# Kernel tuning notes

Measured on AMD Instinct MI355X. Metric: run time of the kernel, lower is better.

Reference implementation:

```python
import jax, jax.numpy as jnp
import numpy as np

N_NODES = 100000
N_EDGES = 1600000
EMB = 64       # embedding_dim
HID = 128      # hidden_channels
N_GRAPHS = 512
N_TASKS = 128
ATOM_VOCAB = 119
BOND_VOCAB = 16


def setup_inputs() -> dict:
    key = jax.random.key(0)
    ks = jax.random.split(key, 24)
    s = 0.02
    inp = {
        'x_idx': jax.random.randint(ks[0], (N_NODES,), 0, ATOM_VOCAB),
        'edge_index': jax.random.randint(ks[1], (2, N_EDGES), 0, N_NODES),
        'edge_attr_idx': jax.random.randint(ks[2], (N_EDGES,), 0, BOND_VOCAB),
        'batch': jnp.sort(jax.random.randint(ks[3], (N_NODES,), 0, N_GRAPHS)),
        'atom_emb': jax.random.normal(ks[4], (ATOM_VOCAB, EMB), jnp.float32) * s,
        'bond_emb': jax.random.normal(ks[5], (BOND_VOCAB, EMB), jnp.float32) * s,
        'w_edge0': jax.random.normal(ks[6], (EMB, EMB), jnp.float32) * s,
        'b_edge0': jnp.zeros((EMB,), jnp.float32),
        'w1_0': jax.random.normal(ks[7], (EMB, HID), jnp.float32) * s,
        'b1_0': jnp.zeros((HID,), jnp.float32),
        'w2_0': jax.random.normal(ks[8], (HID, HID), jnp.float32) * s,
        'b2_0': jnp.zeros((HID,), jnp.float32),
        'w_edge1': jax.random.normal(ks[9], (EMB, HID), jnp.float32) * s,
        'b_edge1': jnp.zeros((HID,), jnp.float32),
        'w1_1': jax.random.normal(ks[10], (HID, HID), jnp.float32) * s,
        'b1_1': jnp.zeros((HID,), jnp.float32),
        'w2_1': jax.random.normal(ks[11], (HID, HID), jnp.float32) * s,
        'b2_1': jnp.zeros((HID,), jnp.float32),
        'lin1_w': jax.random.normal(ks[12], (HID, HID), jnp.float32) * s,
        'lin1_b': jnp.zeros((HID,), jnp.float32),
        'lin2_w': jax.random.normal(ks[13], (HID, N_TASKS), jnp.float32) * s,
        'lin2_b': jnp.zeros((N_TASKS,), jnp.float32),
    }
    return inp


def _gine_conv(x, e, src, dst, we, be, w1, b1, w2, b2):
    # message: relu(x_j + Linear(edge_attr)); aggregate: scatter-add at dst
    msg = jax.nn.relu(x[src] + e @ we + be)            # [E, in_dim]
    agg = jax.ops.segment_sum(msg, dst, num_segments=N_NODES)
    h = x + agg                                        # (1+eps)*x with eps=0
    h = jax.nn.elu(h @ w1 + b1) @ w2 + b2              # GINE nn MLP
    return jax.nn.elu(h)                               # outer F.elu


def reference(x_idx, edge_index, edge_attr_idx, batch,
              atom_emb, bond_emb,
              w_edge0, b_edge0, w1_0, b1_0, w2_0, b2_0,
              w_edge1, b_edge1, w1_1, b1_1, w2_1, b2_1,
              lin1_w, lin1_b, lin2_w, lin2_b):
    x = atom_emb[x_idx]                                # [N, EMB]
    e = bond_emb[edge_attr_idx]                        # [E, EMB]
    src, dst = edge_index[0], edge_index[1]            # flow: source->target
    x = _gine_conv(x, e, src, dst, w_edge0, b_edge0, w1_0, b1_0, w2_0, b2_0)
    x = _gine_conv(x, e, src, dst, w_edge1, b_edge1, w1_1, b1_1, w2_1, b2_1)
    hg = jax.ops.segment_sum(x, batch, num_segments=N_GRAPHS)  # global_add_pool
    hg = jax.nn.relu(hg @ lin1_w + lin1_b)
    return hg @ lin2_w + lin2_b                        # [G, num_tasks]
```

## Files before the change

### kernel.cpp

```cpp
#include <hip/hip_runtime.h>
#include <hip/hip_bf16.h>

static const int NN = 100000;
static const int NE = 1600000;
static const int NG = 512;
static const int NB = 391;
static const int PS = 4608;
static const int CS = 4624;

typedef __attribute__((ext_vector_type(8))) short shortx8;
typedef __attribute__((ext_vector_type(4))) float floatx4;
typedef __attribute__((ext_vector_type(2))) float floatx2;

__device__ __forceinline__ float bf2f(unsigned short u) {
  union { unsigned int i; float f; } v; v.i = ((unsigned int)u) << 16; return v.f;
}
__device__ __forceinline__ unsigned short f2bf(float f) {
  union { float f; unsigned int i; } v; v.f = f;
  return (unsigned short)((v.i + 0x7FFFu + ((v.i >> 16) & 1u)) >> 16);
}
__device__ __forceinline__ float elu_fast(float v) {
  return v > 0.f ? v : (__builtin_amdgcn_exp2f(v * 1.44269504f) - 1.f);
}
__device__ __forceinline__ floatx2 unpk(unsigned int v) {
  union { unsigned int i; float f; } a, b;
  a.i = v << 16; b.i = v & 0xFFFF0000u;
  floatx2 r; r.x = a.f; r.y = b.f; return r;
}

__global__ void k_prep(const float* __restrict__ bond,
                       const float* __restrict__ we0, const float* __restrict__ be0,
                       const float* __restrict__ we1, const float* __restrict__ be1,
                       const float* __restrict__ atom,
                       float* __restrict__ et1, unsigned short* __restrict__ M0,
                       float* __restrict__ hgf, int* __restrict__ bcursor,
                       const float* __restrict__ s0, const float* __restrict__ s1,
                       const float* __restrict__ s2, const float* __restrict__ s3,
                       const float* __restrict__ s4, const float* __restrict__ s5,
                       unsigned short* __restrict__ d0, unsigned short* __restrict__ d1,
                       unsigned short* __restrict__ d2, unsigned short* __restrict__ d3,
                       unsigned short* __restrict__ d4, unsigned short* __restrict__ d5) {
  int blk = blockIdx.x, t = threadIdx.x;
  if (blk < 8) {
    int i = blk * 256 + t;
    int b = i >> 7, c = i & 127;
    float acc = be1[c];
    for (int k = 0; k < 64; ++k) acc += bond[b * 64 + k] * we1[k * 128 + c];
    et1[i] = acc;
  } else if (blk < 484) {
    int i = (blk - 8) * 256 + t;
    int c = i & 63, b = (i >> 6) & 15, a = i >> 10;
    float acc = be0[c];
    for (int k = 0; k < 64; ++k) acc += bond[b * 64 + k] * we0[k * 64 + c];
    acc += atom[a * 64 + c];
    M0[i] = f2bf(acc > 0.f ? acc : 0.f);
  } else if (blk < 868) {
    int task = (blk - 484) >> 6;
    int i = ((blk - 484) & 63) * 256 + t;
    const float* w; unsigned short* wz; int K;
    switch (task) {
      case 0: w = s0; wz = d0; K = 64; break;
      case 1: w = s1; wz = d1; K = 128; break;
      case 2: w = s2; wz = d2; K = 128; break;
      case 3: w = s3; wz = d3; K = 128; break;
      case 4: w = s4; wz = d4; K = 128; break;
      default: w = s5; wz = d5; K = 128; break;
    }
    if (i >= K * 128) return;
    int j = i & 7, lane = (i >> 3) & 63, ct = (i >> 9) & 7, s = i >> 12;
    int k = s * 32 + (lane >> 4) * 8 + j;
    int m = ct * 16 + (lane & 15);
    wz[i] = f2bf(w[k * 128 + m]);
  } else if (blk < 884) {
    int base = (blk - 868) * 4096;
#pragma unroll
    for (int k = 0; k < 16; ++k) hgf[base + k * 256 + t] = 0.f;
  } else {
    if (t < NB) bcursor[t] = t * PS;
    int u = t + 256;
    if (u < NB) bcursor[u] = u * PS;
  }
}

__global__ void k_bin(const int* __restrict__ src, const int* __restrict__ dstp,
                      const int* __restrict__ ea, const int* __restrict__ x_idx,
                      int* __restrict__ bcursor, uint2* __restrict__ pairs) {
  __shared__ int cnt[512];
  __shared__ int incl[512];
  __shared__ int cur[NB];
  __shared__ int rbase[NB];
  __shared__ uint2 stage[4096];
  int t = threadIdx.x;
  int e0 = blockIdx.x * 4096;
  int ecnt = NE - e0; if (ecnt > 4096) ecnt = 4096;
  cnt[t] = 0; cnt[t + 256] = 0;
  __syncthreads();
  for (int k = 0; k < 16; ++k) {
    int i = k * 256 + t;
    if (i < ecnt) atomicAdd(&cnt[dstp[e0 + i] >> 8], 1);
  }
  __syncthreads();
  incl[t] = cnt[t]; incl[t + 256] = cnt[t + 256];
  __syncthreads();
  for (int d = 1; d < 512; d <<= 1) {
    int v0 = (t >= d) ? incl[t - d] : 0;
    int v1 = (t + 256 >= d) ? incl[t + 256 - d] : 0;
    __syncthreads();
    incl[t] += v0; incl[t + 256] += v1;
    __syncthreads();
  }
  if (t < NB) { cur[t] = incl[t] - cnt[t]; if (cnt[t]) rbase[t] = atomicAdd(&bcursor[t], cnt[t]); }
  int u = t + 256;
  if (u < NB) { cur[u] = incl[u] - cnt[u]; if (cnt[u]) rbase[u] = atomicAdd(&bcursor[u], cnt[u]); }
  __syncthreads();
  for (int k = 0; k < 16; ++k) {
    int i = k * 256 + t;
    if (i < ecnt) {
      int e = e0 + i;
      int d = dstp[e];
      int s = src[e];
      unsigned int pk = (unsigned int)s | ((unsigned int)(x_idx[s] * 16 + ea[e]) << 17);
      int p = atomicAdd(&cur[d >> 8], 1);
      stage[p] = make_uint2((unsigned int)d, pk);
    }
  }
  __syncthreads();
  for (int j = t; j < ecnt; j += 256) {
    uint2 p = stage[j];
    int b = (int)(p.x >> 8);
    int excl = incl[b] - cnt[b];
    pairs[rbase[b] + (j - excl)] = p;
  }
}

__global__ void k_fine(const uint2* __restrict__ pairs, const int* __restrict__ bcursor,
                       int* __restrict__ offs, int* __restrict__ cnts,
                       unsigned int* __restrict__ csr0, unsigned int* __restrict__ csr1) {
  __shared__ int cnt[256];
  __shared__ int incl[256];
  __shared__ int cur[256];
  int b = blockIdx.x;
  int t = threadIdx.x;
  int start = b * PS;
  int endv = bcursor[b];
  int cbase = b * CS;
  int base_n = b << 8;
  cnt[t] = 0;
  __syncthreads();
  for (int j = start + t; j < endv; j += 256)
    atomicAdd(&cnt[(int)pairs[j].x - base_n], 1);
  __syncthreads();
  incl[t] = cnt[t];
  __syncthreads();
  for (int d = 1; d < 256; d <<= 1) {
    int v = (t >= d) ? incl[t - d] : 0;
    __syncthreads();
    incl[t] += v;
    __syncthreads();
  }
  int excl = incl[t] - cnt[t];
  cur[t] = excl;
  int node = base_n + t;
  if (node < NN) { offs[node] = cbase + excl; cnts[node] = cnt[t]; }
  __syncthreads();
  for (int j = start + t; j < endv; j += 256) {
    uint2 p = pairs[j];
    int pos = cbase + atomicAdd(&cur[(int)p.x - base_n], 1);
    unsigned int pk = p.y;
    unsigned int idx17 = pk >> 17;
    csr0[pos] = idx17 << 7;
    csr1[pos] = ((pk & 0x1FFFFu) << 8) | (idx17 & 15u);
  }
  __syncthreads();
  int total = incl[255];
  if (t < 16) { csr0[cbase + total + t] = 0u; csr1[cbase + total + t] = 0u; }
}

__global__ __launch_bounds__(256) void k_agg0(
    const int* __restrict__ x_idx, const float* __restrict__ atom,
    const unsigned short* __restrict__ M0, const int* __restrict__ offs,
    const int* __restrict__ cnts,
    const unsigned int* __restrict__ csr0, unsigned short* __restrict__ h0) {
  int t = threadIdx.x, lane = t & 63;
  int half = lane >> 5, c = lane & 31;
  int n = __builtin_amdgcn_readfirstlane(blockIdx.x * 4 + (t >> 6));
  if (n >= NN) return;
  int s = offs[n], e = s + cnts[n];
  const char* Mb = (const char*)M0;
  unsigned int voff = (unsigned int)c * 4u;
  floatx2 acc; acc.x = 0.f; acc.y = 0.f;
  if (half == 0) {
    float2 sv = *(const float2*)((const char*)atom +
                                 ((size_t)(unsigned)x_idx[n] << 8) + (size_t)c * 8u);
    acc.x = sv.x; acc.y = sv.y;
  }
  for (int i = s; i < e; i += 16) {
    unsigned int a0 = csr0[i + 0],  b0 = csr0[i + 1];
    unsigned int a1 = csr0[i + 2],  b1 = csr0[i + 3];
    unsigned int a2 = csr0[i + 4],  b2 = csr0[i + 5];
    unsigned int a3 = csr0[i + 6],  b3 = csr0[i + 7];
    unsigned int a4 = csr0[i + 8],  b4 = csr0[i + 9];
    unsigned int a5 = csr0[i + 10], b5 = csr0[i + 11];
    unsigned int a6 = csr0[i + 12], b6 = csr0[i + 13];
    unsigned int a7 = csr0[i + 14], b7 = csr0[i + 15];
    unsigned int q0 = half ? b0 : a0, q1 = half ? b1 : a1;
    unsigned int q2 = half ? b2 : a2, q3 = half ? b3 : a3;
    unsigned int q4 = half ? b4 : a4, q5 = half ? b5 : a5;
    unsigned int q6 = half ? b6 : a6, q7 = half ? b7 : a7;
    floatx2 m0, m1, m2, m3, m4, m5, m6, m7;
    m0.x = m0.y = (i + 0 + half < e) ? 1.f : 0.f;
    m1.x = m1.y = (i + 2 + half < e) ? 1.f : 0.f;
    m2.x = m2.y = (i + 4 + half < e) ? 1.f : 0.f;
    m3.x = m3.y = (i + 6 + half < e) ? 1.f : 0.f;
    m4.x = m4.y = (i + 8 + half < e) ? 1.f : 0.f;
    m5.x = m5.y = (i + 10 + half < e) ? 1.f : 0.f;
    m6.x = m6.y = (i + 12 + half < e) ? 1.f : 0.f;
    m7.x = m7.y = (i + 14 + half < e) ? 1.f : 0.f;
    unsigned int v0 = *(const unsigned int*)(Mb + q0 + voff);
    unsigned int v1 = *(const unsigned int*)(Mb + q1 + voff);
    unsigned int v2 = *(const unsigned int*)(Mb + q2 + voff);
    unsigned int v3 = *(const unsigned int*)(Mb + q3 + voff);
    unsigned int v4 = *(const unsigned int*)(Mb + q4 + voff);
    unsigned int v5 = *(const unsigned int*)(Mb + q5 + voff);
    unsigned int v6 = *(const unsigned int*)(Mb + q6 + voff);
    unsigned int v7 = *(const unsigned int*)(Mb + q7 + voff);
    acc = __builtin_elementwise_fma(m0, unpk(v0), acc);
    acc = __builtin_elementwise_fma(m1, unpk(v1), acc);
    acc = __builtin_elementwise_fma(m2, unpk(v2), acc);
    acc = __builtin_elementwise_fma(m3, unpk(v3), acc);
    acc = __builtin_elementwise_fma(m4, unpk(v4), acc);
    acc = __builtin_elementwise_fma(m5, unpk(v5), acc);
    acc = __builtin_elementwise_fma(m6, unpk(v6), acc);
    acc = __builtin_elementwise_fma(m7, unpk(v7), acc);
  }
  float ax = acc.x + __shfl_xor(acc.x, 32);
  float ay = acc.y + __shfl_xor(acc.y, 32);
  if (half == 0) {
    unsigned int o = (unsigned int)f2bf(ax) | ((unsigned int)f2bf(ay) << 16);
    *(unsigned int*)(h0 + (size_t)n * 64 + c * 2) = o;
  }
}

__global__ __launch_bounds__(256) void k_agg1(
    const unsigned short* __restrict__ x1, const float* __restrict__ et1,
    const int* __restrict__ offs, const int* __restrict__ cnts,
    const unsigned int* __restrict__ csr1, unsigned short* __restrict__ h1) {
  __shared__ float etl[2048];
  int t = threadIdx.x;
#pragma unroll
  for (int k = 0; k < 8; ++k) etl[k * 256 + t] = et1[k * 256 + t];
  __syncthreads();
  int lane = t & 63;
  int n = __builtin_amdgcn_readfirstlane(blockIdx.x * 4 + (t >> 6));
  if (n >= NN) return;
  int s = offs[n], e = s + cnts[n];
  const char* xb = (const char*)x1;
  unsigned int voff = (unsigned int)lane * 4u;
  const char* etb = (const char*)etl + (size_t)lane * 8u;
  unsigned int xv = *(const unsigned int*)(xb + ((size_t)(unsigned)n << 8) + voff);
  floatx2 acc = unpk(xv);
  floatx2 zero2; zero2.x = 0.f; zero2.y = 0.f;
  for (int i = s; i < e; i += 8) {
    unsigned int q0 = csr1[i + 0], q1 = csr1[i + 1], q2 = csr1[i + 2], q3 = csr1[i + 3];
    unsigned int q4 = csr1[i + 4], q5 = csr1[i + 5], q6 = csr1[i + 6], q7 = csr1[i + 7];
    floatx2 k1, k2, k3, k4, k5, k6, k7;
    k1.x = k1.y = (i + 1 < e) ? 1.f : 0.f;
    k2.x = k2.y = (i + 2 < e) ? 1.f : 0.f;
    k3.x = k3.y = (i + 3 < e) ? 1.f : 0.f;
    k4.x = k4.y = (i + 4 < e) ? 1.f : 0.f;
    k5.x = k5.y = (i + 5 < e) ? 1.f : 0.f;
    k6.x = k6.y = (i + 6 < e) ? 1.f : 0.f;
    k7.x = k7.y = (i + 7 < e) ? 1.f : 0.f;
    unsigned int v0 = *(const unsigned int*)(xb + (q0 & 0xFFFFFF00u) + voff);
    unsigned int v1 = *(const unsigned int*)(xb + (q1 & 0xFFFFFF00u) + voff);
    unsigned int v2 = *(const unsigned int*)(xb + (q2 & 0xFFFFFF00u) + voff);
    unsigned int v3 = *(const unsigned int*)(xb + (q3 & 0xFFFFFF00u) + voff);
    unsigned int v4 = *(const unsigned int*)(xb + (q4 & 0xFFFFFF00u) + voff);
    unsigned int v5 = *(const unsigned int*)(xb + (q5 & 0xFFFFFF00u) + voff);
    unsigned int v6 = *(const unsigned int*)(xb + (q6 & 0xFFFFFF00u) + voff);
    unsigned int v7 = *(const unsigned int*)(xb + (q7 & 0xFFFFFF00u) + voff);
    floatx2 e0 = *(const floatx2*)(etb + ((q0 & 15u) << 9));
    floatx2 e1 = *(const floatx2*)(etb + ((q1 & 15u) << 9));
    floatx2 e2 = *(const floatx2*)(etb + ((q2 & 15u) << 9));
    floatx2 e3 = *(const floatx2*)(etb + ((q3 & 15u) << 9));
    floatx2 e4 = *(const floatx2*)(etb + ((q4 & 15u) << 9));
    floatx2 e5 = *(const floatx2*)(etb + ((q5 & 15u) << 9));
    floatx2 e6 = *(const floatx2*)(etb + ((q6 & 15u) << 9));
    floatx2 e7 = *(const floatx2*)(etb + ((q7 & 15u) << 9));
    acc = acc + __builtin_elementwise_max(unpk(v0) + e0, zero2);
    acc = __builtin_elementwise_fma(k1, __builtin_elementwise_max(unpk(v1) + e1, zero2), acc);
    acc = __builtin_elementwise_fma(k2, __builtin_elementwise_max(unpk(v2) + e2, zero2), acc);
    acc = __builtin_elementwise_fma(k3, __builtin_elementwise_max(unpk(v3) + e3, zero2), acc);
    acc = __builtin_elementwise_fma(k4, __builtin_elementwise_max(unpk(v4) + e4, zero2), acc);
    acc = __builtin_elementwise_fma(k5, __builtin_elementwise_max(unpk(v5) + e5, zero2), acc);
    acc = __builtin_elementwise_fma(k6, __builtin_elementwise_max(unpk(v6) + e6, zero2), acc);
    acc = __builtin_elementwise_fma(k7, __builtin_elementwise_max(unpk(v7) + e7, zero2), acc);
  }
  unsigned int o = (unsigned int)f2bf(acc.x) | ((unsigned int)f2bf(acc.y) << 16);
  *(unsigned int*)(h1 + (size_t)n * 128 + lane * 2) = o;
}

template <int K1>
__global__ __launch_bounds__(256) void k_mlp_t(
    const unsigned short* __restrict__ in,
    const unsigned short* __restrict__ w1z, const float* __restrict__ b1,
    const unsigned short* __restrict__ w2z, const float* __restrict__ b2,
    unsigned short* __restrict__ outb, int N) {
  __shared__ unsigned short tls[4][16][136];
  __shared__ unsigned short b2s[16384];
  int t = threadIdx.x;
  int lane = t & 63;
  int wave = t >> 6;
  int rlo = lane & 15, quad = lane >> 4;

#pragma unroll
  for (int k = 0; k < 8; ++k)
    *(shortx8*)&b2s[(k * 256 + t) * 8] = *(const shortx8*)&w2z[(k * 256 + t) * 8];

  float bm1[8], bm2[8];
#pragma unroll
  for (int ct = 0; ct < 8; ++ct) { bm1[ct] = b1[ct * 16 + rlo]; bm2[ct] = b2[ct * 16 + rlo]; }

  __syncthreads();

#pragma unroll
  for (int t2 = 0; t2 < 2; ++t2) {
    int row0 = blockIdx.x * 128 + t2 * 64 + wave * 16;
    int arow = row0 + rlo;

    floatx4 acc[8];
#pragma unroll
    for (int ct = 0; ct < 8; ++ct) { acc[ct][0]=0.f; acc[ct][1]=0.f; acc[ct][2]=0.f; acc[ct][3]=0.f; }
    const int NS = K1 >> 5;
#pragma unroll
    for (int s = 0; s < NS; ++s) {
      shortx8 a = {0,0,0,0,0,0,0,0};
      if (arow < N) a = *(const shortx8*)(in + (size_t)arow * K1 + s * 32 + quad * 8);
      const unsigned short* wp = w1z + ((size_t)(s * 8) * 64 + lane) * 8;
#pragma unroll
      for (int ct = 0; ct < 8; ++ct) {
        shortx8 b = *(const shortx8*)(wp + ct * 512);
        acc[ct] = __builtin_amdgcn_mfma_f32_16x16x32_bf16(a, b, acc[ct], 0, 0, 0);
      }
    }
#pragma unroll
    for (int ct = 0; ct < 8; ++ct) {
#pragma unroll
      for (int r = 0; r < 4; ++r) {
        float v = elu_fast(acc[ct][r] + bm1[ct]);
        tls[wave][quad * 4 + r][ct * 16 + rlo] = f2bf(v);
      }
    }

    floatx4 acc2[8];
#pragma unroll
    for (int ct = 0; ct < 8; ++ct) { acc2[ct][0]=0.f; acc2[ct][1]=0.f; acc2[ct][2]=0.f; acc2[ct][3]=0.f; }
#pragma unroll
    for (int s = 0; s < 4; ++s) {
      shortx8 a = *(const shortx8*)&tls[wave][rlo][s * 32 + quad * 8];
      const unsigned short* wp = &b2s[((s * 8) * 64 + lane) * 8];
#pragma unroll
      for (int ct = 0; ct < 8; ++ct) {
        shortx8 b = *(const shortx8*)(wp + ct * 512);
        acc2[ct] = __builtin_amdgcn_mfma_f32_16x16x32_bf16(a, b, acc2[ct], 0, 0, 0);
      }
    }
#pragma unroll
    for (int ct = 0; ct < 8; ++ct) {
#pragma unroll
      for (int r = 0; r < 4; ++r) {
        float v = elu_fast(acc2[ct][r] + bm2[ct]);
        tls[wave][quad * 4 + r][ct * 16 + rlo] = f2bf(v);
      }
    }
    int srow = lane >> 2;
    int schunk = lane & 3;
    int grow = row0 + srow;
#pragma unroll
    for (int k = 0; k < 4; ++k) {
      int ch = schunk + k * 4;
      if (grow < N)
        *(shortx8*)(outb + (size_t)grow * 128 + ch * 8) =
            *(const shortx8*)&tls[wave][srow][ch * 8];
    }
  }
}

__global__ __launch_bounds__(256) void k_pool(
    const unsigned short* __restrict__ x2, const int* __restrict__ batch,
    float* __restrict__ hgf) {
  int gt = blockIdx.x * 256 + threadIdx.x;
  int chunk = gt >> 6, lane = gt & 63;
  int n0 = chunk * 32;
  if (n0 >= NN) return;
  int nend = n0 + 32; if (nend > NN) nend = NN;
  float ax = 0.f, ay = 0.f;
  const unsigned short* xp = x2 + lane * 2;
  int gcur = batch[n0];
  for (int n = n0; n < nend; ++n) {
    int g = batch[n];
    if (g != gcur) {
      atomicAdd(&hgf[gcur * 128 + lane * 2], ax);
      atomicAdd(&hgf[gcur * 128 + lane * 2 + 1], ay);
      ax = 0.f; ay = 0.f; gcur = g;
    }
    unsigned int v = *(const unsigned int*)(xp + (size_t)n * 128);
    ax += bf2f((unsigned short)(v & 0xFFFF));
    ay += bf2f((unsigned short)(v >> 16));
  }
  atomicAdd(&hgf[gcur * 128 + lane * 2], ax);
  atomicAdd(&hgf[gcur * 128 + lane * 2 + 1], ay);
}

__global__ void k_head(const float* __restrict__ in,
                       const unsigned short* __restrict__ w1z, const float* __restrict__ b1,
                       const unsigned short* __restrict__ w2z, const float* __restrict__ b2,
                       float* __restrict__ outf, int N) {
  __shared__ unsigned short tls[4][16][136];
  int lane = threadIdx.x & 63;
  int wave = threadIdx.x >> 6;
  int row0 = blockIdx.x * 64 + wave * 16;
  int rlo = lane & 15, quad = lane >> 4;
  int arow = row0 + rlo;
  floatx4 acc[8];
#pragma unroll
  for (int ct = 0; ct < 8; ++ct) { acc[ct][0]=0.f; acc[ct][1]=0.f; acc[ct][2]=0.f; acc[ct][3]=0.f; }
#pragma unroll
  for (int s = 0; s < 4; ++s) {
    shortx8 a = {0,0,0,0,0,0,0,0};
    if (arow < N) {
      const float* rp = in + (size_t)arow * 128 + s * 32 + quad * 8;
      float4 f0 = *(const float4*)rp;
      float4 f1 = *(const float4*)(rp + 4);
      a[0] = (short)f2bf(f0.x); a[1] = (short)f2bf(f0.y);
      a[2] = (short)f2bf(f0.z); a[3] = (short)f2bf(f0.w);
      a[4] = (short)f2bf(f1.x); a[5] = (short)f2bf(f1.y);
      a[6] = (short)f2bf(f1.z); a[7] = (short)f2bf(f1.w);
    }
    const unsigned short* wp = w1z + ((size_t)(s * 8) * 64 + lane) * 8;
#pragma unroll
    for (int ct = 0; ct < 8; ++ct) {
      shortx8 b = *(const shortx8*)(wp + ct * 512);
      acc[ct] = __builtin_amdgcn_mfma_f32_16x16x32_bf16(a, b, acc[ct], 0, 0, 0);
    }
  }
#pragma unroll
  for (int ct = 0; ct < 8; ++ct) {
    float bm = b1[ct * 16 + rlo];
#pragma unroll
    for (int r = 0; r < 4; ++r) {
      float v = acc[ct][r] + bm;
      v = v > 0.f ? v : 0.f;
      tls[wave][quad * 4 + r][ct * 16 + rlo] = f2bf(v);
    }
  }
  __syncthreads();
  floatx4 acc2[8];
#pragma unroll
  for (int ct = 0; ct < 8; ++ct) { acc2[ct][0]=0.f; acc2[ct][1]=0.f; acc2[ct][2]=0.f; acc2[ct][3]=0.f; }
#pragma unroll
  for (int s = 0; s < 4; ++s) {
    shortx8 a = *(const shortx8*)&tls[wave][rlo][s * 32 + quad * 8];
    const unsigned short* wp = w2z + ((size_t)(s * 8) * 64 + lane) * 8;
#pragma unroll
    for (int ct = 0; ct < 8; ++ct) {
      shortx8 b = *(const shortx8*)(wp + ct * 512);
      acc2[ct] = __builtin_amdgcn_mfma_f32_16x16x32_bf16(a, b, acc2[ct], 0, 0, 0);
    }
  }
#pragma unroll
  for (int ct = 0; ct < 8; ++ct) {
    float bm = b2[ct * 16 + rlo];
#pragma unroll
    for (int r = 0; r < 4; ++r) {
      int rr = row0 + quad * 4 + r;
      if (rr < N) outf[(size_t)rr * 128 + ct * 16 + rlo] = acc2[ct][r] + bm;
    }
  }
}

extern "C" void kernel_launch(void* const* d_in, const int* in_sizes, int n_in,
                              void* d_out, int out_size, void* d_ws, size_t ws_size,
                              hipStream_t stream) {
  const int* x_idx  = (const int*)d_in[0];
  const int* e_src  = (const int*)d_in[1];
  const int* e_dst  = e_src + NE;
  const int* e_attr = (const int*)d_in[2];
  const int* batch  = (const int*)d_in[3];
  const float* atom = (const float*)d_in[4];
  const float* bond = (const float*)d_in[5];
  const float* we0  = (const float*)d_in[6];
  const float* be0  = (const float*)d_in[7];
  const float* w1_0 = (const float*)d_in[8];
  const float* b1_0 = (const float*)d_in[9];
  const float* w2_0 = (const float*)d_in[10];
  const float* b2_0 = (const float*)d_in[11];
  const float* we1  = (const float*)d_in[12];
  const float* be1  = (const float*)d_in[13];
  const float* w1_1 = (const float*)d_in[14];
  const float* b1_1 = (const float*)d_in[15];
  const float* w2_1 = (const float*)d_in[16];
  const float* b2_1 = (const float*)d_in[17];
  const float* l1w  = (const float*)d_in[18];
  const float* l1b  = (const float*)d_in[19];
  const float* l2w  = (const float*)d_in[20];
  const float* l2b  = (const float*)d_in[21];

  char* ws = (char*)d_ws;
  size_t off = 0;
  auto alloc = [&](size_t bytes) -> void* {
    void* p = ws + off;
    off = (off + bytes + 255) & ~(size_t)255;
    return p;
  };
  int* bcursor = (int*)alloc((size_t)NB * 4);
  int* offs    = (int*)alloc((size_t)NN * 4);
  int* cnts    = (int*)alloc((size_t)NN * 4);
  float* et1   = (float*)alloc(16 * 128 * 4);
  unsigned short* M0 = (unsigned short*)alloc((size_t)1904 * 64 * 2);
  float* hgf   = (float*)alloc((size_t)NG * 128 * 4);
  unsigned short* w1_0z = (unsigned short*)alloc(64 * 128 * 2);
  unsigned short* w2_0z = (unsigned short*)alloc(128 * 128 * 2);
  unsigned short* w1_1z = (unsigned short*)alloc(128 * 128 * 2);
  unsigned short* w2_1z = (unsigned short*)alloc(128 * 128 * 2);
  unsigned short* l1z   = (unsigned short*)alloc(128 * 128 * 2);
  unsigned short* l2z   = (unsigned short*)alloc(128 * 128 * 2);
  uint2* pairs = (uint2*)alloc((size_t)NB * PS * 8);
  unsigned int* csr0 = (unsigned int*)alloc((size_t)NB * CS * 4);
  unsigned int* csr1 = (unsigned int*)alloc((size_t)NB * CS * 4);
  unsigned short* x1 = (unsigned short*)alloc((size_t)NN * 128 * 2);
  unsigned short* h1 = (unsigned short*)alloc((size_t)NN * 128 * 2);
  unsigned short* h0 = (unsigned short*)pairs;
  unsigned short* x2 = h1;

  k_prep<<<885, 256, 0, stream>>>(bond, we0, be0, we1, be1, atom, et1, M0, hgf, bcursor,
                                  w1_0, w2_0, w1_1, w2_1, l1w, l2w,
                                  w1_0z, w2_0z, w1_1z, w2_1z, l1z, l2z);
  k_bin<<<(NE + 4095) / 4096, 256, 0, stream>>>(e_src, e_dst, e_attr, x_idx, bcursor, pairs);
  k_fine<<<NB, 256, 0, stream>>>(pairs, bcursor, offs, cnts, csr0, csr1);
  k_agg0<<<NN / 4, 256, 0, stream>>>(x_idx, atom, M0, offs, cnts, csr0, h0);
  k_mlp_t<64><<<(NN + 127) / 128, 256, 0, stream>>>(h0, w1_0z, b1_0, w2_0z, b2_0, x1, NN);
  k_agg1<<<NN / 4, 256, 0, stream>>>(x1, et1, offs, cnts, csr1, h1);
  k_mlp_t<128><<<(NN + 127) / 128, 256, 0, stream>>>(h1, w1_1z, b1_1, w2_1z, b2_1, x2, NN);
  k_pool<<<(((NN + 31) / 32) * 64 + 255) / 256, 256, 0, stream>>>(x2, batch, hgf);
  k_head<<<(NG + 63) / 64, 256, 0, stream>>>(hgf, l1z, l1b, l2z, l2b, (float*)d_out, NG);
}
```

Before: 323.3 us.

## Widen gather loads to 16 bytes per lane in edge aggregation kernels

Both aggregation kernels now have each lane load 16 bytes (8 bf16 values) of a neighbour row instead of 4 bytes. Several edges are processed in parallel across lane groups (8 groups in layer 0, 4 in layer 1), and the partial sums are combined with cross-lane shuffles. The edge-embedding table in shared memory is re-laid out with padding so the wider reads avoid bank conflicts. The aim is fewer, wider memory transactions and more edges in flight per wave, at the cost of extra shuffle reductions and more wasted lanes on nodes with few edges.

```diff
diff --git a/kernel.cpp b/kernel.cpp
--- a/kernel.cpp
+++ b/kernel.cpp
@@ -182,122 +182,133 @@
     const int* __restrict__ cnts,
     const unsigned int* __restrict__ csr0, unsigned short* __restrict__ h0) {
   int t = threadIdx.x, lane = t & 63;
-  int half = lane >> 5, c = lane & 31;
+  int oct = lane >> 3, cl = lane & 7;
   int n = __builtin_amdgcn_readfirstlane(blockIdx.x * 4 + (t >> 6));
   if (n >= NN) return;
   int s = offs[n], e = s + cnts[n];
   const char* Mb = (const char*)M0;
-  unsigned int voff = (unsigned int)c * 4u;
-  floatx2 acc; acc.x = 0.f; acc.y = 0.f;
-  if (half == 0) {
-    float2 sv = *(const float2*)((const char*)atom +
-                                 ((size_t)(unsigned)x_idx[n] << 8) + (size_t)c * 8u);
-    acc.x = sv.x; acc.y = sv.y;
-  }
-  for (int i = s; i < e; i += 16) {
-    unsigned int a0 = csr0[i + 0],  b0 = csr0[i + 1];
-    unsigned int a1 = csr0[i + 2],  b1 = csr0[i + 3];
-    unsigned int a2 = csr0[i + 4],  b2 = csr0[i + 5];
-    unsigned int a3 = csr0[i + 6],  b3 = csr0[i + 7];
-    unsigned int a4 = csr0[i + 8],  b4 = csr0[i + 9];
-    unsigned int a5 = csr0[i + 10], b5 = csr0[i + 11];
-    unsigned int a6 = csr0[i + 12], b6 = csr0[i + 13];
-    unsigned int a7 = csr0[i + 14], b7 = csr0[i + 15];
-    unsigned int q0 = half ? b0 : a0, q1 = half ? b1 : a1;
-    unsigned int q2 = half ? b2 : a2, q3 = half ? b3 : a3;
-    unsigned int q4 = half ? b4 : a4, q5 = half ? b5 : a5;
-    unsigned int q6 = half ? b6 : a6, q7 = half ? b7 : a7;
-    floatx2 m0, m1, m2, m3, m4, m5, m6, m7;
-    m0.x = m0.y = (i + 0 + half < e) ? 1.f : 0.f;
-    m1.x = m1.y = (i + 2 + half < e) ? 1.f : 0.f;
-    m2.x = m2.y = (i + 4 + half < e) ? 1.f : 0.f;
-    m3.x = m3.y = (i + 6 + half < e) ? 1.f : 0.f;
-    m4.x = m4.y = (i + 8 + half < e) ? 1.f : 0.f;
-    m5.x = m5.y = (i + 10 + half < e) ? 1.f : 0.f;
-    m6.x = m6.y = (i + 12 + half < e) ? 1.f : 0.f;
-    m7.x = m7.y = (i + 14 + half < e) ? 1.f : 0.f;
-    unsigned int v0 = *(const unsigned int*)(Mb + q0 + voff);
-    unsigned int v1 = *(const unsigned int*)(Mb + q1 + voff);
-    unsigned int v2 = *(const unsigned int*)(Mb + q2 + voff);
-    unsigned int v3 = *(const unsigned int*)(Mb + q3 + voff);
-    unsigned int v4 = *(const unsigned int*)(Mb + q4 + voff);
-    unsigned int v5 = *(const unsigned int*)(Mb + q5 + voff);
-    unsigned int v6 = *(const unsigned int*)(Mb + q6 + voff);
-    unsigned int v7 = *(const unsigned int*)(Mb + q7 + voff);
-    acc = __builtin_elementwise_fma(m0, unpk(v0), acc);
-    acc = __builtin_elementwise_fma(m1, unpk(v1), acc);
-    acc = __builtin_elementwise_fma(m2, unpk(v2), acc);
-    acc = __builtin_elementwise_fma(m3, unpk(v3), acc);
-    acc = __builtin_elementwise_fma(m4, unpk(v4), acc);
-    acc = __builtin_elementwise_fma(m5, unpk(v5), acc);
-    acc = __builtin_elementwise_fma(m6, unpk(v6), acc);
-    acc = __builtin_elementwise_fma(m7, unpk(v7), acc);
-  }
-  float ax = acc.x + __shfl_xor(acc.x, 32);
-  float ay = acc.y + __shfl_xor(acc.y, 32);
-  if (half == 0) {
-    unsigned int o = (unsigned int)f2bf(ax) | ((unsigned int)f2bf(ay) << 16);
-    *(unsigned int*)(h0 + (size_t)n * 64 + c * 2) = o;
-  }
+  unsigned int claneoff = (unsigned int)(cl * 16);
+  floatx2 a0, a1, a2, a3;
+  a0.x = a0.y = a1.x = a1.y = a2.x = a2.y = a3.x = a3.y = 0.f;
+  if (oct == 0) {
+    const float* ap = atom + ((size_t)(unsigned)x_idx[n] << 6) + (cl << 3);
+    float4 f0 = *(const float4*)ap;
+    float4 f1 = *(const float4*)(ap + 4);
+    a0.x = f0.x; a0.y = f0.y; a1.x = f0.z; a1.y = f0.w;
+    a2.x = f1.x; a2.y = f1.y; a3.x = f1.z; a3.y = f1.w;
+  }
+  const unsigned int* cp = csr0 + s + oct;
+  for (int r = e - s; r > 0; r -= 16, cp += 16) {
+    unsigned int qA = cp[0];
+    unsigned int qB = cp[8];
+    float mA = (oct < r) ? 1.f : 0.f;
+    float mB = (oct + 8 < r) ? 1.f : 0.f;
+    floatx2 mA2; mA2.x = mA; mA2.y = mA;
+    floatx2 mB2; mB2.x = mB; mB2.y = mB;
+    uint4 vA = *(const uint4*)(Mb + (size_t)(qA | claneoff));
+    uint4 vB = *(const uint4*)(Mb + (size_t)(qB | claneoff));
+    a0 = __builtin_elementwise_fma(mA2, unpk(vA.x), a0);
+    a1 = __builtin_elementwise_fma(mA2, unpk(vA.y), a1);
+    a2 = __builtin_elementwise_fma(mA2, unpk(vA.z), a2);
+    a3 = __builtin_elementwise_fma(mA2, unpk(vA.w), a3);
+    a0 = __builtin_elementwise_fma(mB2, unpk(vB.x), a0);
+    a1 = __builtin_elementwise_fma(mB2, unpk(vB.y), a1);
+    a2 = __builtin_elementwise_fma(mB2, unpk(vB.z), a2);
+    a3 = __builtin_elementwise_fma(mB2, unpk(vB.w), a3);
+  }
+  a0.x += __shfl_xor(a0.x, 8);  a0.y += __shfl_xor(a0.y, 8);
+  a1.x += __shfl_xor(a1.x, 8);  a1.y += __shfl_xor(a1.y, 8);
+  a2.x += __shfl_xor(a2.x, 8);  a2.y += __shfl_xor(a2.y, 8);
+  a3.x += __shfl_xor(a3.x, 8);  a3.y += __shfl_xor(a3.y, 8);
+  a0.x += __shfl_xor(a0.x, 16); a0.y += __shfl_xor(a0.y, 16);
+  a1.x += __shfl_xor(a1.x, 16); a1.y += __shfl_xor(a1.y, 16);
+  a2.x += __shfl_xor(a2.x, 16); a2.y += __shfl_xor(a2.y, 16);
+  a3.x += __shfl_xor(a3.x, 16); a3.y += __shfl_xor(a3.y, 16);
+  a0.x += __shfl_xor(a0.x, 32); a0.y += __shfl_xor(a0.y, 32);
+  a1.x += __shfl_xor(a1.x, 32); a1.y += __shfl_xor(a1.y, 32);
+  a2.x += __shfl_xor(a2.x, 32); a2.y += __shfl_xor(a2.y, 32);
+  a3.x += __shfl_xor(a3.x, 32); a3.y += __shfl_xor(a3.y, 32);
+  if (oct == 0) {
+    uint4 o;
+    o.x = (unsigned int)f2bf(a0.x) | ((unsigned int)f2bf(a0.y) << 16);
+    o.y = (unsigned int)f2bf(a1.x) | ((unsigned int)f2bf(a1.y) << 16);
+    o.z = (unsigned int)f2bf(a2.x) | ((unsigned int)f2bf(a2.y) << 16);
+    o.w = (unsigned int)f2bf(a3.x) | ((unsigned int)f2bf(a3.y) << 16);
+    *(uint4*)((char*)h0 + ((size_t)n << 7) + claneoff) = o;
+  }
+}
+
+__device__ __forceinline__ void upd1(unsigned int q, float m,
+    const char* xb, const char* etb, unsigned int claneoff,
+    floatx2& a0, floatx2& a1, floatx2& a2, floatx2& a3) {
+  floatx2 mm; mm.x = m; mm.y = m;
+  floatx2 z2; z2.x = 0.f; z2.y = 0.f;
+  uint4 v = *(const uint4*)(xb + (size_t)((q & 0xFFFFFF00u) | claneoff));
+  const char* ee = etb + (q & 15u) * 560u;
+  floatx4 ef0 = *(const floatx4*)(ee);
+  floatx4 ef1 = *(const floatx4*)(ee + 16);
+  floatx2 e0; e0.x = ef0.x; e0.y = ef0.y;
+  floatx2 e1; e1.x = ef0.z; e1.y = ef0.w;
+  floatx2 e2; e2.x = ef1.x; e2.y = ef1.y;
+  floatx2 e3; e3.x = ef1.z; e3.y = ef1.w;
+  a0 = __builtin_elementwise_fma(mm, __builtin_elementwise_max(unpk(v.x) + e0, z2), a0);
+  a1 = __builtin_elementwise_fma(mm, __builtin_elementwise_max(unpk(v.y) + e1, z2), a1);
+  a2 = __builtin_elementwise_fma(mm, __builtin_elementwise_max(unpk(v.z) + e2, z2), a2);
+  a3 = __builtin_elementwise_fma(mm, __builtin_elementwise_max(unpk(v.w) + e3, z2), a3);
 }
 
 __global__ __launch_bounds__(256) void k_agg1(
     const unsigned short* __restrict__ x1, const float* __restrict__ et1,
     const int* __restrict__ offs, const int* __restrict__ cnts,
     const unsigned int* __restrict__ csr1, unsigned short* __restrict__ h1) {
-  __shared__ float etl[2048];
+  __shared__ float etl[16 * 140];
   int t = threadIdx.x;
 #pragma unroll
-  for (int k = 0; k < 8; ++k) etl[k * 256 + t] = et1[k * 256 + t];
+  for (int k = 0; k < 8; ++k) {
+    int idx = k * 256 + t;
+    int b = idx >> 7, c = idx & 127;
+    etl[b * 140 + c + ((c >> 5) << 2)] = et1[idx];
+  }
   __syncthreads();
   int lane = t & 63;
+  int qtr = lane >> 4, cl = lane & 15;
   int n = __builtin_amdgcn_readfirstlane(blockIdx.x * 4 + (t >> 6));
   if (n >= NN) return;
   int s = offs[n], e = s + cnts[n];
   const char* xb = (const char*)x1;
-  unsigned int voff = (unsigned int)lane * 4u;
-  const char* etb = (const char*)etl + (size_t)lane * 8u;
-  unsigned int xv = *(const unsigned int*)(xb + ((size_t)(unsigned)n << 8) + voff);
-  floatx2 acc = unpk(xv);
-  floatx2 zero2; zero2.x = 0.f; zero2.y = 0.f;
-  for (int i = s; i < e; i += 8) {
-    unsigned int q0 = csr1[i + 0], q1 = csr1[i + 1], q2 = csr1[i + 2], q3 = csr1[i + 3];
-    unsigned int q4 = csr1[i + 4], q5 = csr1[i + 5], q6 = csr1[i + 6], q7 = csr1[i + 7];
-    floatx2 k1, k2, k3, k4, k5, k6, k7;
-    k1.x = k1.y = (i + 1 < e) ? 1.f : 0.f;
-    k2.x = k2.y = (i + 2 < e) ? 1.f : 0.f;
-    k3.x = k3.y = (i + 3 < e) ? 1.f : 0.f;
-    k4.x = k4.y = (i + 4 < e) ? 1.f : 0.f;
-    k5.x = k5.y = (i + 5 < e) ? 1.f : 0.f;
-    k6.x = k6.y = (i + 6 < e) ? 1.f : 0.f;
-    k7.x = k7.y = (i + 7 < e) ? 1.f : 0.f;
-    unsigned int v0 = *(const unsigned int*)(xb + (q0 & 0xFFFFFF00u) + voff);
-    unsigned int v1 = *(const unsigned int*)(xb + (q1 & 0xFFFFFF00u) + voff);
-    unsigned int v2 = *(const unsigned int*)(xb + (q2 & 0xFFFFFF00u) + voff);
-    unsigned int v3 = *(const unsigned int*)(xb + (q3 & 0xFFFFFF00u) + voff);
-    unsigned int v4 = *(const unsigned int*)(xb + (q4 & 0xFFFFFF00u) + voff);
-    unsigned int v5 = *(const unsigned int*)(xb + (q5 & 0xFFFFFF00u) + voff);
-    unsigned int v6 = *(const unsigned int*)(xb + (q6 & 0xFFFFFF00u) + voff);
-    unsigned int v7 = *(const unsigned int*)(xb + (q7 & 0xFFFFFF00u) + voff);
-    floatx2 e0 = *(const floatx2*)(etb + ((q0 & 15u) << 9));
-    floatx2 e1 = *(const floatx2*)(etb + ((q1 & 15u) << 9));
-    floatx2 e2 = *(const floatx2*)(etb + ((q2 & 15u) << 9));
-    floatx2 e3 = *(const floatx2*)(etb + ((q3 & 15u) << 9));
-    floatx2 e4 = *(const floatx2*)(etb + ((q4 & 15u) << 9));
-    floatx2 e5 = *(const floatx2*)(etb + ((q5 & 15u) << 9));
-    floatx2 e6 = *(const floatx2*)(etb + ((q6 & 15u) << 9));
-    floatx2 e7 = *(const floatx2*)(etb + ((q7 & 15u) << 9));
-    acc = acc + __builtin_elementwise_max(unpk(v0) + e0, zero2);
-    acc = __builtin_elementwise_fma(k1, __builtin_elementwise_max(unpk(v1) + e1, zero2), acc);
-    acc = __builtin_elementwise_fma(k2, __builtin_elementwise_max(unpk(v2) + e2, zero2), acc);
-    acc = __builtin_elementwise_fma(k3, __builtin_elementwise_max(unpk(v3) + e3, zero2), acc);
-    acc = __builtin_elementwise_fma(k4, __builtin_elementwise_max(unpk(v4) + e4, zero2), acc);
-    acc = __builtin_elementwise_fma(k5, __builtin_elementwise_max(unpk(v5) + e5, zero2), acc);
-    acc = __builtin_elementwise_fma(k6, __builtin_elementwise_max(unpk(v6) + e6, zero2), acc);
-    acc = __builtin_elementwise_fma(k7, __builtin_elementwise_max(unpk(v7) + e7, zero2), acc);
-  }
-  unsigned int o = (unsigned int)f2bf(acc.x) | ((unsigned int)f2bf(acc.y) << 16);
-  *(unsigned int*)(h1 + (size_t)n * 128 + lane * 2) = o;
+  const char* etb = (const char*)etl + (size_t)(cl * 32 + ((cl >> 2) << 4));
+  unsigned int claneoff = (unsigned int)(cl * 16);
+  floatx2 a0, a1, a2, a3;
+  a0.x = a0.y = a1.x = a1.y = a2.x = a2.y = a3.x = a3.y = 0.f;
+  if (qtr == 0) {
+    uint4 v = *(const uint4*)(xb + ((size_t)(unsigned)n << 8) + claneoff);
+    a0 = unpk(v.x); a1 = unpk(v.y); a2 = unpk(v.z); a3 = unpk(v.w);
+  }
+  const unsigned int* cp = csr1 + s + qtr;
+  for (int r = e - s; r > 0; r -= 8, cp += 8) {
+    unsigned int qA = cp[0];
+    unsigned int qB = cp[4];
+    float mA = (qtr < r) ? 1.f : 0.f;
+    float mB = (qtr + 4 < r) ? 1.f : 0.f;
+    upd1(qA, mA, xb, etb, claneoff, a0, a1, a2, a3);
+    upd1(qB, mB, xb, etb, claneoff, a0, a1, a2, a3);
+  }
+  a0.x += __shfl_xor(a0.x, 16); a0.y += __shfl_xor(a0.y, 16);
+  a1.x += __shfl_xor(a1.x, 16); a1.y += __shfl_xor(a1.y, 16);
+  a2.x += __shfl_xor(a2.x, 16); a2.y += __shfl_xor(a2.y, 16);
+  a3.x += __shfl_xor(a3.x, 16); a3.y += __shfl_xor(a3.y, 16);
+  a0.x += __shfl_xor(a0.x, 32); a0.y += __shfl_xor(a0.y, 32);
+  a1.x += __shfl_xor(a1.x, 32); a1.y += __shfl_xor(a1.y, 32);
+  a2.x += __shfl_xor(a2.x, 32); a2.y += __shfl_xor(a2.y, 32);
+  a3.x += __shfl_xor(a3.x, 32); a3.y += __shfl_xor(a3.y, 32);
+  if (qtr == 0) {
+    uint4 o;
+    o.x = (unsigned int)f2bf(a0.x) | ((unsigned int)f2bf(a0.y) << 16);
+    o.y = (unsigned int)f2bf(a1.x) | ((unsigned int)f2bf(a1.y) << 16);
+    o.z = (unsigned int)f2bf(a2.x) | ((unsigned int)f2bf(a2.y) << 16);
+    o.w = (unsigned int)f2bf(a3.x) | ((unsigned int)f2bf(a3.y) << 16);
+    *(uint4*)((char*)h1 + ((size_t)n << 8) + claneoff) = o;
+  }
 }
 
 template <int K1>
```

Result: slower. 334.6 us (+3.5%).

## Pad per-node CSR segments to multiples of 8 with neutral sentinel edges

Applied to the files above, without the earlier changes.

Each node's CSR segment is padded to a multiple of 8 entries, and the padding points to sentinel rows: a zero row in M0 and a row of bf16 -inf in x1. With that, the aggregation kernels no longer need per-edge validity masks. k_agg0 switches from 16-wide to 8-wide iterations with plain adds, and k_agg1 drops its mask FMAs. The cost is a larger CSR buffer (CS raised to 6400), extra padding writes in k_fine, and gathers spent on padded entries, up to 7 per node.

```diff
diff --git a/kernel.cpp b/kernel.cpp
--- a/kernel.cpp
+++ b/kernel.cpp
@@ -6,7 +6,7 @@
 static const int NG = 512;
 static const int NB = 391;
 static const int PS = 4608;
-static const int CS = 4624;
+static const int CS = 6400;
 
 typedef __attribute__((ext_vector_type(8))) short shortx8;
 typedef __attribute__((ext_vector_type(4))) float floatx4;
@@ -34,6 +34,7 @@
                        const float* __restrict__ atom,
                        float* __restrict__ et1, unsigned short* __restrict__ M0,
                        float* __restrict__ hgf, int* __restrict__ bcursor,
+                       unsigned short* __restrict__ x1s,
                        const float* __restrict__ s0, const float* __restrict__ s1,
                        const float* __restrict__ s2, const float* __restrict__ s3,
                        const float* __restrict__ s4, const float* __restrict__ s5,
@@ -79,6 +80,8 @@
     if (t < NB) bcursor[t] = t * PS;
     int u = t + 256;
     if (u < NB) bcursor[u] = u * PS;
+    if (t < 32) ((unsigned int*)(M0 + 1904 * 64))[t] = 0u;
+    if (t < 64) ((unsigned int*)(x1s + (size_t)NN * 128))[t] = 0xFF80FF80u;
   }
 }
 
@@ -150,7 +153,9 @@
   for (int j = start + t; j < endv; j += 256)
     atomicAdd(&cnt[(int)pairs[j].x - base_n], 1);
   __syncthreads();
-  incl[t] = cnt[t];
+  int myc = cnt[t];
+  int myp = (myc + 7) & ~7;
+  incl[t] = myp;
   __syncthreads();
   for (int d = 1; d < 256; d <<= 1) {
     int v = (t >= d) ? incl[t - d] : 0;
@@ -158,10 +163,10 @@
     incl[t] += v;
     __syncthreads();
   }
-  int excl = incl[t] - cnt[t];
+  int excl = incl[t] - myp;
   cur[t] = excl;
   int node = base_n + t;
-  if (node < NN) { offs[node] = cbase + excl; cnts[node] = cnt[t]; }
+  if (node < NN) { offs[node] = cbase + excl; cnts[node] = myc; }
   __syncthreads();
   for (int j = start + t; j < endv; j += 256) {
     uint2 p = pairs[j];
@@ -172,8 +177,11 @@
     csr1[pos] = ((pk & 0x1FFFFu) << 8) | (idx17 & 15u);
   }
   __syncthreads();
-  int total = incl[255];
-  if (t < 16) { csr0[cbase + total + t] = 0u; csr1[cbase + total + t] = 0u; }
+  for (int j = myc; j < myp; ++j) {
+    int pos = cbase + excl + j;
+    csr0[pos] = (unsigned int)(1904 << 7);
+    csr1[pos] = ((unsigned int)NN) << 8;
+  }
 }
 
 __global__ __launch_bounds__(256) void k_agg0(
@@ -185,7 +193,8 @@
   int half = lane >> 5, c = lane & 31;
   int n = __builtin_amdgcn_readfirstlane(blockIdx.x * 4 + (t >> 6));
   if (n >= NN) return;
-  int s = offs[n], e = s + cnts[n];
+  int s = offs[n];
+  int ep = s + ((cnts[n] + 7) & ~7);
   const char* Mb = (const char*)M0;
   unsigned int voff = (unsigned int)c * 4u;
   floatx2 acc; acc.x = 0.f; acc.y = 0.f;
@@ -194,44 +203,21 @@
                                  ((size_t)(unsigned)x_idx[n] << 8) + (size_t)c * 8u);
     acc.x = sv.x; acc.y = sv.y;
   }
-  for (int i = s; i < e; i += 16) {
-    unsigned int a0 = csr0[i + 0],  b0 = csr0[i + 1];
-    unsigned int a1 = csr0[i + 2],  b1 = csr0[i + 3];
-    unsigned int a2 = csr0[i + 4],  b2 = csr0[i + 5];
-    unsigned int a3 = csr0[i + 6],  b3 = csr0[i + 7];
-    unsigned int a4 = csr0[i + 8],  b4 = csr0[i + 9];
-    unsigned int a5 = csr0[i + 10], b5 = csr0[i + 11];
-    unsigned int a6 = csr0[i + 12], b6 = csr0[i + 13];
-    unsigned int a7 = csr0[i + 14], b7 = csr0[i + 15];
+  for (int i = s; i < ep; i += 8) {
+    unsigned int a0 = csr0[i + 0], b0 = csr0[i + 1];
+    unsigned int a1 = csr0[i + 2], b1 = csr0[i + 3];
+    unsigned int a2 = csr0[i + 4], b2 = csr0[i + 5];
+    unsigned int a3 = csr0[i + 6], b3 = csr0[i + 7];
     unsigned int q0 = half ? b0 : a0, q1 = half ? b1 : a1;
     unsigned int q2 = half ? b2 : a2, q3 = half ? b3 : a3;
-    unsigned int q4 = half ? b4 : a4, q5 = half ? b5 : a5;
-    unsigned int q6 = half ? b6 : a6, q7 = half ? b7 : a7;
-    floatx2 m0, m1, m2, m3, m4, m5, m6, m7;
-    m0.x = m0.y = (i + 0 + half < e) ? 1.f : 0.f;
-    m1.x = m1.y = (i + 2 + half < e) ? 1.f : 0.f;
-    m2.x = m2.y = (i + 4 + half < e) ? 1.f : 0.f;
-    m3.x = m3.y = (i + 6 + half < e) ? 1.f : 0.f;
-    m4.x = m4.y = (i + 8 + half < e) ? 1.f : 0.f;
-    m5.x = m5.y = (i + 10 + half < e) ? 1.f : 0.f;
-    m6.x = m6.y = (i + 12 + half < e) ? 1.f : 0.f;
-    m7.x = m7.y = (i + 14 + half < e) ? 1.f : 0.f;
     unsigned int v0 = *(const unsigned int*)(Mb + q0 + voff);
     unsigned int v1 = *(const unsigned int*)(Mb + q1 + voff);
     unsigned int v2 = *(const unsigned int*)(Mb + q2 + voff);
     unsigned int v3 = *(const unsigned int*)(Mb + q3 + voff);
-    unsigned int v4 = *(const unsigned int*)(Mb + q4 + voff);
-    unsigned int v5 = *(const unsigned int*)(Mb + q5 + voff);
-    unsigned int v6 = *(const unsigned int*)(Mb + q6 + voff);
-    unsigned int v7 = *(const unsigned int*)(Mb + q7 + voff);
-    acc = __builtin_elementwise_fma(m0, unpk(v0), acc);
-    acc = __builtin_elementwise_fma(m1, unpk(v1), acc);
-    acc = __builtin_elementwise_fma(m2, unpk(v2), acc);
-    acc = __builtin_elementwise_fma(m3, unpk(v3), acc);
-    acc = __builtin_elementwise_fma(m4, unpk(v4), acc);
-    acc = __builtin_elementwise_fma(m5, unpk(v5), acc);
-    acc = __builtin_elementwise_fma(m6, unpk(v6), acc);
-    acc = __builtin_elementwise_fma(m7, unpk(v7), acc);
+    acc = acc + unpk(v0);
+    acc = acc + unpk(v1);
+    acc = acc + unpk(v2);
+    acc = acc + unpk(v3);
   }
   float ax = acc.x + __shfl_xor(acc.x, 32);
   float ay = acc.y + __shfl_xor(acc.y, 32);
@@ -253,32 +239,25 @@
   int lane = t & 63;
   int n = __builtin_amdgcn_readfirstlane(blockIdx.x * 4 + (t >> 6));
   if (n >= NN) return;
-  int s = offs[n], e = s + cnts[n];
+  int s = offs[n];
+  int ep = s + ((cnts[n] + 7) & ~7);
   const char* xb = (const char*)x1;
   unsigned int voff = (unsigned int)lane * 4u;
   const char* etb = (const char*)etl + (size_t)lane * 8u;
   unsigned int xv = *(const unsigned int*)(xb + ((size_t)(unsigned)n << 8) + voff);
   floatx2 acc = unpk(xv);
   floatx2 zero2; zero2.x = 0.f; zero2.y = 0.f;
-  for (int i = s; i < e; i += 8) {
+  for (int i = s; i < ep; i += 8) {
     unsigned int q0 = csr1[i + 0], q1 = csr1[i + 1], q2 = csr1[i + 2], q3 = csr1[i + 3];
     unsigned int q4 = csr1[i + 4], q5 = csr1[i + 5], q6 = csr1[i + 6], q7 = csr1[i + 7];
-    floatx2 k1, k2, k3, k4, k5, k6, k7;
-    k1.x = k1.y = (i + 1 < e) ? 1.f : 0.f;
-    k2.x = k2.y = (i + 2 < e) ? 1.f : 0.f;
-    k3.x = k3.y = (i + 3 < e) ? 1.f : 0.f;
-    k4.x = k4.y = (i + 4 < e) ? 1.f : 0.f;
-    k5.x = k5.y = (i + 5 < e) ? 1.f : 0.f;
-    k6.x = k6.y = (i + 6 < e) ? 1.f : 0.f;
-    k7.x = k7.y = (i + 7 < e) ? 1.f : 0.f;
-    unsigned int v0 = *(const unsigned int*)(xb + (q0 & 0xFFFFFF00u) + voff);
-    unsigned int v1 = *(const unsigned int*)(xb + (q1 & 0xFFFFFF00u) + voff);
-    unsigned int v2 = *(const unsigned int*)(xb + (q2 & 0xFFFFFF00u) + voff);
-    unsigned int v3 = *(const unsigned int*)(xb + (q3 & 0xFFFFFF00u) + voff);
-    unsigned int v4 = *(const unsigned int*)(xb + (q4 & 0xFFFFFF00u) + voff);
-    unsigned int v5 = *(const unsigned int*)(xb + (q5 & 0xFFFFFF00u) + voff);
-    unsigned int v6 = *(const unsigned int*)(xb + (q6 & 0xFFFFFF00u) + voff);
-    unsigned int v7 = *(const unsigned int*)(xb + (q7 & 0xFFFFFF00u) + voff);
+    unsigned int v0 = *(const unsigned int*)(xb + ((q0 & 0xFFFFFF00u) | voff));
+    unsigned int v1 = *(const unsigned int*)(xb + ((q1 & 0xFFFFFF00u) | voff));
+    unsigned int v2 = *(const unsigned int*)(xb + ((q2 & 0xFFFFFF00u) | voff));
+    unsigned int v3 = *(const unsigned int*)(xb + ((q3 & 0xFFFFFF00u) | voff));
+    unsigned int v4 = *(const unsigned int*)(xb + ((q4 & 0xFFFFFF00u) | voff));
+    unsigned int v5 = *(const unsigned int*)(xb + ((q5 & 0xFFFFFF00u) | voff));
+    unsigned int v6 = *(const unsigned int*)(xb + ((q6 & 0xFFFFFF00u) | voff));
+    unsigned int v7 = *(const unsigned int*)(xb + ((q7 & 0xFFFFFF00u) | voff));
     floatx2 e0 = *(const floatx2*)(etb + ((q0 & 15u) << 9));
     floatx2 e1 = *(const floatx2*)(etb + ((q1 & 15u) << 9));
     floatx2 e2 = *(const floatx2*)(etb + ((q2 & 15u) << 9));
@@ -288,13 +267,13 @@
     floatx2 e6 = *(const floatx2*)(etb + ((q6 & 15u) << 9));
     floatx2 e7 = *(const floatx2*)(etb + ((q7 & 15u) << 9));
     acc = acc + __builtin_elementwise_max(unpk(v0) + e0, zero2);
-    acc = __builtin_elementwise_fma(k1, __builtin_elementwise_max(unpk(v1) + e1, zero2), acc);
-    acc = __builtin_elementwise_fma(k2, __builtin_elementwise_max(unpk(v2) + e2, zero2), acc);
-    acc = __builtin_elementwise_fma(k3, __builtin_elementwise_max(unpk(v3) + e3, zero2), acc);
-    acc = __builtin_elementwise_fma(k4, __builtin_elementwise_max(unpk(v4) + e4, zero2), acc);
-    acc = __builtin_elementwise_fma(k5, __builtin_elementwise_max(unpk(v5) + e5, zero2), acc);
-    acc = __builtin_elementwise_fma(k6, __builtin_elementwise_max(unpk(v6) + e6, zero2), acc);
-    acc = __builtin_elementwise_fma(k7, __builtin_elementwise_max(unpk(v7) + e7, zero2), acc);
+    acc = acc + __builtin_elementwise_max(unpk(v1) + e1, zero2);
+    acc = acc + __builtin_elementwise_max(unpk(v2) + e2, zero2);
+    acc = acc + __builtin_elementwise_max(unpk(v3) + e3, zero2);
+    acc = acc + __builtin_elementwise_max(unpk(v4) + e4, zero2);
+    acc = acc + __builtin_elementwise_max(unpk(v5) + e5, zero2);
+    acc = acc + __builtin_elementwise_max(unpk(v6) + e6, zero2);
+    acc = acc + __builtin_elementwise_max(unpk(v7) + e7, zero2);
   }
   unsigned int o = (unsigned int)f2bf(acc.x) | ((unsigned int)f2bf(acc.y) << 16);
   *(unsigned int*)(h1 + (size_t)n * 128 + lane * 2) = o;
@@ -517,7 +496,7 @@
   int* offs    = (int*)alloc((size_t)NN * 4);
   int* cnts    = (int*)alloc((size_t)NN * 4);
   float* et1   = (float*)alloc(16 * 128 * 4);
-  unsigned short* M0 = (unsigned short*)alloc((size_t)1904 * 64 * 2);
+  unsigned short* M0 = (unsigned short*)alloc((size_t)1905 * 64 * 2);
   float* hgf   = (float*)alloc((size_t)NG * 128 * 4);
   unsigned short* w1_0z = (unsigned short*)alloc(64 * 128 * 2);
   unsigned short* w2_0z = (unsigned short*)alloc(128 * 128 * 2);
@@ -528,12 +507,13 @@
   uint2* pairs = (uint2*)alloc((size_t)NB * PS * 8);
   unsigned int* csr0 = (unsigned int*)alloc((size_t)NB * CS * 4);
   unsigned int* csr1 = (unsigned int*)alloc((size_t)NB * CS * 4);
-  unsigned short* x1 = (unsigned short*)alloc((size_t)NN * 128 * 2);
+  unsigned short* x1 = (unsigned short*)alloc((size_t)(NN + 1) * 128 * 2);
   unsigned short* h1 = (unsigned short*)alloc((size_t)NN * 128 * 2);
   unsigned short* h0 = (unsigned short*)pairs;
   unsigned short* x2 = h1;
 
   k_prep<<<885, 256, 0, stream>>>(bond, we0, be0, we1, be1, atom, et1, M0, hgf, bcursor,
+                                  x1,
                                   w1_0, w2_0, w1_1, w2_1, l1w, l2w,
                                   w1_0z, w2_0z, w1_1z, w2_1z, l1z, l2z);
   k_bin<<<(NE + 4095) / 4096, 256, 0, stream>>>(e_src, e_dst, e_attr, x_idx, bcursor, pairs);
```

New measurement: 328.1 us. Within noise of the previous version (+1.5%).
